# Kernel tuning notes

Hardware: AMD Instinct MI355X
Metric: run time of the kernel (lower is better)

Reference implementation:

```python
import jax, jax.numpy as jnp
import numpy as np

B, T, D = 4, 2048, 1024
E, K = 8, 2
H = int(D * 2.0)  # d_hidden


def setup_inputs() -> dict:
    key = jax.random.key(0)
    ks = jax.random.split(key, 7)
    x = jax.random.normal(ks[0], (B, T, D), dtype=jnp.float32)
    # router Linear(d_model, n_experts)
    router_w = jax.random.normal(ks[1], (D, E), dtype=jnp.float32) * (1.0 / np.sqrt(D))
    router_b = jnp.zeros((E,), dtype=jnp.float32)
    # expert weights, xavier_uniform-like scale
    lim1 = float(np.sqrt(6.0 / (D + H)))
    lim2 = float(np.sqrt(6.0 / (H + D)))
    w1 = jax.random.uniform(ks[2], (E, D, H), dtype=jnp.float32, minval=-lim1, maxval=lim1)
    b1 = jnp.zeros((E, H), dtype=jnp.float32)
    w2 = jax.random.uniform(ks[3], (E, H, D), dtype=jnp.float32, minval=-lim2, maxval=lim2)
    b2 = jnp.zeros((E, D), dtype=jnp.float32)
    return {"x": x, "router_w": router_w, "router_b": router_b,
            "w1": w1, "b1": b1, "w2": w2, "b2": b2}


def reference(x, router_w, router_b, w1, b1, w2, b2):
    Bs, Ts, d = x.shape
    N = Bs * Ts
    h = x.reshape(N, d)
    logits = h @ router_w + router_b                      # [N, E]
    probs = jax.nn.softmax(logits, axis=-1)
    weights, indices = jax.lax.top_k(probs, K)            # [N, K]
    weights = weights / (jnp.sum(weights, axis=-1, keepdims=True) + 1e-9)
    rows = jnp.arange(N)[:, None]
    # routing mask M and combine weights G (scatter over expert axis)
    M = jnp.zeros((N, E), dtype=bool).at[rows, indices].set(True)
    G = jnp.zeros((N, E), dtype=x.dtype).at[rows, indices].add(weights)
    # dense expert compute; tokens with G[:,e]==0 contribute nothing,
    # matching the masked gather/scatter loop exactly (dropout=0, eval mode)
    hidden = jax.nn.gelu(jnp.einsum('nd,edh->enh', h, w1) + b1[:, None, :],
                         approximate=False)               # [E, N, H]
    expert_out = jnp.einsum('enh,ehd->end', hidden, w2) + b2[:, None, :]  # [E, N, D]
    y = jnp.einsum('ne,end->nd', G, expert_out)           # combine
    y = y.reshape(Bs, Ts, d)
    # aux losses
    f_e = M.astype(jnp.float32).mean(axis=0)
    P_e = probs.mean(axis=0)
    lb_loss = -E * jnp.sum(f_e * P_e)
    z = jax.nn.logsumexp(logits, axis=-1)
    z_loss = jnp.mean(z ** 2)
    entropy = jnp.mean(-jnp.sum(probs * jnp.log(probs + 1e-10), axis=-1))
    return (y, lb_loss, z_loss, entropy, f_e, P_e)
```

## Files before the change

### kernel.cpp

```cpp
#include <hip/hip_runtime.h>
#include <hip/hip_bf16.h>

#define NTOK 8192
#define DM 1024
#define NE 8
#define DH 2048
#define CAP 18432

typedef __attribute__((ext_vector_type(8))) short short8;
typedef __attribute__((ext_vector_type(4))) float float4v;

#define ASYNC_COPY16(gsrc, ldst)                                                              \
    __builtin_amdgcn_global_load_lds((const __attribute__((address_space(1))) unsigned int*)(gsrc), \
                                     (__attribute__((address_space(3))) unsigned int*)(ldst), \
                                     16, 0, 0)

static __device__ __forceinline__ unsigned short f2bf(float f) {
    __hip_bfloat16 h = __float2bfloat16(f);
    return *reinterpret_cast<unsigned short*>(&h);
}

static __device__ __forceinline__ float fast_gelu(float v) {
    float x = v * 0.70710678118654752f;
    float ax = fabsf(x);
    float t = __frcp_rn(1.0f + 0.3275911f * ax);
    float poly = ((((1.061405429f * t - 1.453152027f) * t + 1.421413741f) * t
                   - 0.284496736f) * t + 0.254829592f) * t;
    float y = 1.0f - poly * __expf(-ax * ax);
    float erfv = copysignf(y, x);
    return 0.5f * v * (1.0f + erfv);
}


__global__ __launch_bounds__(256) void k_transpose(const float* __restrict__ src,
                                                   __hip_bfloat16* __restrict__ dst,
                                                   int R, int C) {
    __shared__ float t[64][65];
    size_t mat = (size_t)blockIdx.z * R * C;
    src += mat;
    dst += mat;
    int c0 = blockIdx.x * 64, r0 = blockIdx.y * 64;
    int tx = threadIdx.x & 63, ty = threadIdx.x >> 6;
#pragma unroll
    for (int i = 0; i < 16; i++) {
        int r = ty + i * 4;
        t[r][tx] = src[(size_t)(r0 + r) * C + c0 + tx];
    }
    __syncthreads();
    int rx = (threadIdx.x & 15) * 4;
    int cy = threadIdx.x >> 4;
#pragma unroll
    for (int i = 0; i < 4; i++) {
        int c = cy + i * 16;
        ushort4 v;
        v.x = f2bf(t[rx + 0][c]);
        v.y = f2bf(t[rx + 1][c]);
        v.z = f2bf(t[rx + 2][c]);
        v.w = f2bf(t[rx + 3][c]);
        *(ushort4*)((unsigned short*)dst + (size_t)(c0 + c) * R + r0 + rx) = v;
    }
}


__global__ __launch_bounds__(256) void k_router(const float* __restrict__ x,
                                                const float* __restrict__ rw,
                                                const float* __restrict__ rb,
                                                __hip_bfloat16* __restrict__ xb,
                                                int* __restrict__ topidx,
                                                float* __restrict__ topw,
                                                float* __restrict__ probs8,
                                                float* __restrict__ zent) {
    int lane = threadIdx.x & 63, wv = threadIdx.x >> 6;
    int n = blockIdx.x * 4 + wv;
    const float* xr = x + (size_t)n * DM;
    unsigned short* xbr = (unsigned short*)xb + (size_t)n * DM;
    float p[8] = {0.f, 0.f, 0.f, 0.f, 0.f, 0.f, 0.f, 0.f};
#pragma unroll
    for (int i = 0; i < 16; i++) {
        int d = lane + i * 64;
        float xv = xr[d];
        xbr[d] = f2bf(xv);
        const float4* w4 = (const float4*)(rw + (size_t)d * 8);
        float4 wa = w4[0], wb = w4[1];
        p[0] += xv * wa.x; p[1] += xv * wa.y; p[2] += xv * wa.z; p[3] += xv * wa.w;
        p[4] += xv * wb.x; p[5] += xv * wb.y; p[6] += xv * wb.z; p[7] += xv * wb.w;
    }
#pragma unroll
    for (int e = 0; e < 8; e++) {
#pragma unroll
        for (int off = 32; off > 0; off >>= 1) p[e] += __shfl_down(p[e], off);
    }
    if (lane == 0) {
        float logits[8], probs[8];
        float mx = -1e30f;
#pragma unroll
        for (int e = 0; e < 8; e++) {
            logits[e] = p[e] + rb[e];
            mx = fmaxf(mx, logits[e]);
        }
        float se = 0.f;
#pragma unroll
        for (int e = 0; e < 8; e++) {
            probs[e] = __expf(logits[e] - mx);
            se += probs[e];
        }
        float inv = 1.f / se;
        float z = mx + logf(se);
        float ent = 0.f;
#pragma unroll
        for (int e = 0; e < 8; e++) {
            probs[e] *= inv;
            ent -= probs[e] * logf(probs[e] + 1e-10f);
        }
        int i0 = 0;
#pragma unroll
        for (int e = 1; e < 8; e++)
            if (probs[e] > probs[i0]) i0 = e;
        int i1 = (i0 == 0) ? 1 : 0;
#pragma unroll
        for (int e = 0; e < 8; e++)
            if (e != i0 && e != i1 && probs[e] > probs[i1]) i1 = e;
        float w0 = probs[i0], w1v = probs[i1];
        float s = w0 + w1v + 1e-9f;
        topidx[2 * n] = i0;
        topidx[2 * n + 1] = i1;
        topw[2 * n] = w0 / s;
        topw[2 * n + 1] = w1v / s;
        float* pr = probs8 + (size_t)n * 8;
#pragma unroll
        for (int e = 0; e < 8; e++) pr[e] = probs[e];
        zent[2 * n] = z * z;
        zent[2 * n + 1] = ent;
    }
}


__global__ __launch_bounds__(256) void k_stats(const int* __restrict__ topidx,
                                               const float* __restrict__ probs8,
                                               const float* __restrict__ zent,
                                               float* __restrict__ fcnt,
                                               float* __restrict__ sump,
                                               float* __restrict__ szent) {
    int n = blockIdx.x * 256 + threadIdx.x;
    float v[18];
    int e0 = topidx[2 * n], e1 = topidx[2 * n + 1];
#pragma unroll
    for (int e = 0; e < 8; e++) v[e] = (float)((e == e0) + (e == e1));
    const float4* p4 = (const float4*)(probs8 + (size_t)n * 8);
    float4 pa = p4[0], pb = p4[1];
    v[8] = pa.x; v[9] = pa.y; v[10] = pa.z; v[11] = pa.w;
    v[12] = pb.x; v[13] = pb.y; v[14] = pb.z; v[15] = pb.w;
    v[16] = zent[2 * n];
    v[17] = zent[2 * n + 1];
#pragma unroll
    for (int i = 0; i < 18; i++)
#pragma unroll
        for (int off = 32; off > 0; off >>= 1) v[i] += __shfl_down(v[i], off);
    __shared__ float part[4][18];
    int lane = threadIdx.x & 63, wv = threadIdx.x >> 6;
    if (lane == 0)
#pragma unroll
        for (int i = 0; i < 18; i++) part[wv][i] = v[i];
    __syncthreads();
    if (threadIdx.x == 0) {
#pragma unroll
        for (int i = 0; i < 18; i++) {
            float s = part[0][i] + part[1][i] + part[2][i] + part[3][i];
            if (i < 8) atomicAdd(&fcnt[i], s);
            else if (i < 16) atomicAdd(&sump[i - 8], s);
            else atomicAdd(&szent[i - 16], s);
        }
    }
}


__global__ void k_scan(const float* __restrict__ fcnt, int* __restrict__ offs) {
    if (threadIdx.x == 0 && blockIdx.x == 0) {
        int o = 0;
        for (int e = 0; e < NE; e++) {
            offs[e] = o;
            int c = (int)(fcnt[e] + 0.5f);
            o += (c + 255) & ~255;
        }
        offs[NE] = o;
    }
}

__global__ __launch_bounds__(256) void k_scatter(const int* __restrict__ topidx,
                                                 const float* __restrict__ topw,
                                                 const int* __restrict__ offs,
                                                 int* __restrict__ cnt2,
                                                 int* __restrict__ rowtok,
                                                 float* __restrict__ roww,
                                                 int* __restrict__ slot) {
    __shared__ int lcnt[8], lbase[8];
    int tid = threadIdx.x;
    if (tid < 8) lcnt[tid] = 0;
    __syncthreads();
    int n = blockIdx.x * 256 + tid;
    int e0 = topidx[2 * n], e1 = topidx[2 * n + 1];
    int p0 = atomicAdd(&lcnt[e0], 1);
    int p1 = atomicAdd(&lcnt[e1], 1);
    __syncthreads();
    if (tid < 8) lbase[tid] = atomicAdd(&cnt2[tid], lcnt[tid]);
    __syncthreads();
    int r0 = offs[e0] + lbase[e0] + p0;
    int r1 = offs[e1] + lbase[e1] + p1;
    rowtok[r0] = n; roww[r0] = topw[2 * n];     slot[2 * n] = r0;
    rowtok[r1] = n; roww[r1] = topw[2 * n + 1]; slot[2 * n + 1] = r1;
}


#define KT1 (DM / 32)

__global__ __launch_bounds__(512) void k_gemm1(const __hip_bfloat16* __restrict__ xb,
                                               const __hip_bfloat16* __restrict__ w1T,
                                               const float* __restrict__ b1,
                                               const int* __restrict__ rowtok,
                                               const int* __restrict__ offs,
                                               __hip_bfloat16* __restrict__ hid) {
    int bid = blockIdx.x;
    int ib = bid >> 3;
    int row0 = ((bid & 7) * 9 + (ib >> 3)) * 256;
    if (row0 >= offs[NE]) return;
    int h0 = (ib & 7) * 256;
    int e = 0;
    while (row0 >= offs[e + 1]) e++;
    int tid = threadIdx.x;

    __shared__ __align__(16) short lds[3][16384];

    int sr = tid >> 2;
    int pc = tid & 3;
    int ch = pc ^ ((sr >> 1) & 3);
    int t0 = rowtok[row0 + sr];
    int t1 = rowtok[row0 + 128 + sr];
    const short* aS0 = (const short*)xb + (size_t)(t0 < 0 ? 0 : t0) * DM + ch * 8;
    const short* aS1 = (const short*)xb + (size_t)(t1 < 0 ? 0 : t1) * DM + ch * 8;
    const short* bS0 = (const short*)w1T + ((size_t)e * DH + h0 + sr) * DM + ch * 8;
    const short* bS1 = (const short*)w1T + ((size_t)e * DH + h0 + 128 + sr) * DM + ch * 8;
    int ldo = sr * 32 + pc * 8;

    int lane = tid & 63, wv = tid >> 6;
    int wm = (wv >> 2) * 128, wn = (wv & 3) * 64;
    int quad = lane >> 4, l16 = lane & 15;
    int a_off[8], b_off[4];
#pragma unroll
    for (int mt = 0; mt < 8; mt++) {
        int r = wm + mt * 16 + l16;
        a_off[mt] = r * 32 + ((quad ^ ((r >> 1) & 3)) * 8);
    }
#pragma unroll
    for (int nt = 0; nt < 4; nt++) {
        int r = wn + nt * 16 + l16;
        b_off[nt] = 8192 + r * 32 + ((quad ^ ((r >> 1) & 3)) * 8);
    }
    float4v acc[8][4];
#pragma unroll
    for (int i = 0; i < 8; i++)
#pragma unroll
        for (int j = 0; j < 4; j++) {
            float4v z = {0.f, 0.f, 0.f, 0.f};
            acc[i][j] = z;
        }

    ASYNC_COPY16(aS0, &lds[0][ldo]);
    ASYNC_COPY16(aS1, &lds[0][4096 + ldo]);
    ASYNC_COPY16(bS0, &lds[0][8192 + ldo]);
    ASYNC_COPY16(bS1, &lds[0][12288 + ldo]);
    ASYNC_COPY16(aS0 + 32, &lds[1][ldo]);
    ASYNC_COPY16(aS1 + 32, &lds[1][4096 + ldo]);
    ASYNC_COPY16(bS0 + 32, &lds[1][8192 + ldo]);
    ASYNC_COPY16(bS1 + 32, &lds[1][12288 + ldo]);
    asm volatile("s_waitcnt vmcnt(4)" ::: "memory");
    asm volatile("s_barrier" ::: "memory");

    int bi = 0;
#pragma unroll 1
    for (int t = 0; t < KT1; ++t) {
        const short* Ab = &lds[bi][0];
        int sbi = bi + 2; if (sbi >= 3) sbi -= 3;
        int k2 = (t + 2) * 32;
        short8 bf[4], af[4];
#pragma unroll
        for (int nt = 0; nt < 4; nt++) bf[nt] = *(const short8*)(Ab + b_off[nt]);
#pragma unroll
        for (int mt = 0; mt < 4; mt++) af[mt] = *(const short8*)(Ab + a_off[mt]);
        if (t + 2 < KT1) {
            ASYNC_COPY16(aS0 + k2, &lds[sbi][ldo]);
            ASYNC_COPY16(bS0 + k2, &lds[sbi][8192 + ldo]);
        }
        asm volatile("s_barrier" ::: "memory");
        __builtin_amdgcn_sched_barrier(0);
        __builtin_amdgcn_s_setprio(1);
#pragma unroll
        for (int mt = 0; mt < 4; mt++)
#pragma unroll
            for (int nt = 0; nt < 4; nt++)
                acc[mt][nt] = __builtin_amdgcn_mfma_f32_16x16x32_bf16(af[mt], bf[nt], acc[mt][nt], 0, 0, 0);
        __builtin_amdgcn_s_setprio(0);
        __builtin_amdgcn_sched_barrier(0);
        asm volatile("s_barrier" ::: "memory");
#pragma unroll
        for (int mt = 0; mt < 4; mt++) af[mt] = *(const short8*)(Ab + a_off[4 + mt]);
        if (t + 2 < KT1) {
            ASYNC_COPY16(aS1 + k2, &lds[sbi][4096 + ldo]);
            ASYNC_COPY16(bS1 + k2, &lds[sbi][12288 + ldo]);
        }
        asm volatile("s_barrier" ::: "memory");
        __builtin_amdgcn_sched_barrier(0);
        __builtin_amdgcn_s_setprio(1);
#pragma unroll
        for (int mt = 0; mt < 4; mt++)
#pragma unroll
            for (int nt = 0; nt < 4; nt++)
                acc[4 + mt][nt] = __builtin_amdgcn_mfma_f32_16x16x32_bf16(af[mt], bf[nt], acc[4 + mt][nt], 0, 0, 0);
        __builtin_amdgcn_s_setprio(0);
        __builtin_amdgcn_sched_barrier(0);
        if (t + 2 < KT1) asm volatile("s_waitcnt vmcnt(4)" ::: "memory");
        else             asm volatile("s_waitcnt vmcnt(0)" ::: "memory");
        asm volatile("s_barrier" ::: "memory");
        bi++; if (bi == 3) bi = 0;
    }

    const float* b1e = b1 + (size_t)e * DH + h0;
#pragma unroll
    for (int mt = 0; mt < 8; mt++) {
#pragma unroll
        for (int nt = 0; nt < 4; nt++) {
            int rl = wm + mt * 16 + quad * 4;
            int cl = wn + nt * 16 + l16;
            float bias = b1e[cl];
#pragma unroll
            for (int r = 0; r < 4; r++) {
                float v = fast_gelu(acc[mt][nt][r] + bias);
                hid[(size_t)(row0 + rl + r) * DH + h0 + cl] = __float2bfloat16(v);
            }
        }
    }
}


#define KT2 (DH / 32)

__global__ __launch_bounds__(512) void k_gemm2(const __hip_bfloat16* __restrict__ hid,
                                               const __hip_bfloat16* __restrict__ w2T,
                                               const float* __restrict__ b2,
                                               const float* __restrict__ roww,
                                               const int* __restrict__ offs,
                                               float* __restrict__ outb) {
    int bid = blockIdx.x;
    int ib = bid >> 3;
    int row0 = ((bid & 7) * 9 + (ib >> 3)) * 256;
    if (row0 >= offs[NE]) return;
    int d0 = (ib & 7) * 128;
    int e = 0;
    while (row0 >= offs[e + 1]) e++;
    int tid = threadIdx.x;

    __shared__ __align__(16) short lds[3][12288];

    int sr = tid >> 2, pc = tid & 3;
    int ch = pc ^ ((sr >> 1) & 3);
    const short* aS0 = (const short*)hid + (size_t)(row0 + sr) * DH + ch * 8;
    const short* aS1 = (const short*)hid + (size_t)(row0 + 128 + sr) * DH + ch * 8;
    const short* bS  = (const short*)w2T + ((size_t)e * DM + d0 + sr) * DH + ch * 8;
    int ldo = sr * 32 + pc * 8;

    int lane = tid & 63, wv = tid >> 6;
    int wm = (wv >> 1) * 64, wn = (wv & 1) * 64;
    int quad = lane >> 4, l16 = lane & 15;
    int a_off[4], b_off[4];
#pragma unroll
    for (int mt = 0; mt < 4; mt++) {
        int r = wm + mt * 16 + l16;
        a_off[mt] = r * 32 + ((quad ^ ((r >> 1) & 3)) * 8);
    }
#pragma unroll
    for (int nt = 0; nt < 4; nt++) {
        int r = wn + nt * 16 + l16;
        b_off[nt] = 8192 + r * 32 + ((quad ^ ((r >> 1) & 3)) * 8);
    }
    float4v acc[4][4];
#pragma unroll
    for (int i = 0; i < 4; i++)
#pragma unroll
        for (int j = 0; j < 4; j++) {
            float4v z = {0.f, 0.f, 0.f, 0.f};
            acc[i][j] = z;
        }

    ASYNC_COPY16(aS0, &lds[0][ldo]);
    ASYNC_COPY16(aS1, &lds[0][4096 + ldo]);
    ASYNC_COPY16(bS,  &lds[0][8192 + ldo]);
    ASYNC_COPY16(aS0 + 32, &lds[1][ldo]);
    ASYNC_COPY16(aS1 + 32, &lds[1][4096 + ldo]);
    ASYNC_COPY16(bS + 32,  &lds[1][8192 + ldo]);
    asm volatile("s_waitcnt vmcnt(3)" ::: "memory");
    asm volatile("s_barrier" ::: "memory");

    int bi = 0;
#pragma unroll 1
    for (int t = 0; t < KT2; ++t) {
        const short* Ab = &lds[bi][0];
        int sbi = bi + 2; if (sbi >= 3) sbi -= 3;
        int k2 = (t + 2) * 32;
        short8 af[4], bf[4];
#pragma unroll
        for (int mt = 0; mt < 4; mt++) af[mt] = *(const short8*)(Ab + a_off[mt]);
#pragma unroll
        for (int nt = 0; nt < 4; nt++) bf[nt] = *(const short8*)(Ab + b_off[nt]);
        if (t + 2 < KT2) {
            ASYNC_COPY16(aS0 + k2, &lds[sbi][ldo]);
            ASYNC_COPY16(aS1 + k2, &lds[sbi][4096 + ldo]);
            ASYNC_COPY16(bS + k2,  &lds[sbi][8192 + ldo]);
        }
        asm volatile("s_barrier" ::: "memory");
        __builtin_amdgcn_sched_barrier(0);
        __builtin_amdgcn_s_setprio(1);
#pragma unroll
        for (int mt = 0; mt < 4; mt++)
#pragma unroll
            for (int nt = 0; nt < 4; nt++)
                acc[mt][nt] = __builtin_amdgcn_mfma_f32_16x16x32_bf16(af[mt], bf[nt], acc[mt][nt], 0, 0, 0);
        __builtin_amdgcn_s_setprio(0);
        __builtin_amdgcn_sched_barrier(0);
        if (t + 2 < KT2) asm volatile("s_waitcnt vmcnt(3)" ::: "memory");
        else             asm volatile("s_waitcnt vmcnt(0)" ::: "memory");
        asm volatile("s_barrier" ::: "memory");
        bi++; if (bi == 3) bi = 0;
    }

    const float* b2e = b2 + (size_t)e * DM + d0;
#pragma unroll
    for (int mt = 0; mt < 4; mt++) {
#pragma unroll
        for (int nt = 0; nt < 4; nt++) {
            int rl = wm + mt * 16 + quad * 4;
            int cl = wn + nt * 16 + l16;
            float bias = b2e[cl];
#pragma unroll
            for (int r = 0; r < 4; r++) {
                int grow = row0 + rl + r;
                float v = (acc[mt][nt][r] + bias) * roww[grow];
                outb[(size_t)grow * DM + d0 + cl] = v;
            }
        }
    }
}


__global__ __launch_bounds__(256) void k_combine(const float* __restrict__ outb,
                                                 const int* __restrict__ slot,
                                                 float* __restrict__ y) {
    int n = blockIdx.x;
    int r0 = slot[2 * n], r1 = slot[2 * n + 1];
    const float4* p0 = (const float4*)(outb + (size_t)r0 * DM);
    const float4* p1 = (const float4*)(outb + (size_t)r1 * DM);
    float4 a = p0[threadIdx.x], b = p1[threadIdx.x];
    float4 c;
    c.x = a.x + b.x;
    c.y = a.y + b.y;
    c.z = a.z + b.z;
    c.w = a.w + b.w;
    ((float4*)(y + (size_t)n * DM))[threadIdx.x] = c;
}

__global__ void k_finalize(const float* __restrict__ fcnt, const float* __restrict__ sump,
                           const float* __restrict__ szent, float* __restrict__ out) {
    if (threadIdx.x == 0 && blockIdx.x == 0) {
        const float invN = 1.0f / (float)NTOK;
        float lb = 0.f;
        float f[NE], P[NE];
        for (int e = 0; e < NE; e++) {
            f[e] = fcnt[e] * invN;
            P[e] = sump[e] * invN;
            lb += f[e] * P[e];
        }
        size_t base = (size_t)NTOK * DM;
        out[base + 0] = -(float)NE * lb;
        out[base + 1] = szent[0] * invN;
        out[base + 2] = szent[1] * invN;
        for (int e = 0; e < NE; e++) out[base + 3 + e] = f[e];
        for (int e = 0; e < NE; e++) out[base + 11 + e] = P[e];
    }
}


extern "C" void kernel_launch(void* const* d_in, const int* in_sizes, int n_in,
                              void* d_out, int out_size, void* d_ws, size_t ws_size,
                              hipStream_t stream) {
    const float* x  = (const float*)d_in[0];
    const float* rw = (const float*)d_in[1];
    const float* rb = (const float*)d_in[2];
    const float* w1 = (const float*)d_in[3];
    const float* b1 = (const float*)d_in[4];
    const float* w2 = (const float*)d_in[5];
    const float* b2 = (const float*)d_in[6];
    float* out = (float*)d_out;

    char* ws = (char*)d_ws;
    size_t o = 0;
    auto alloc = [&](size_t bytes) {
        size_t r = o;
        o = (o + bytes + 255) & ~(size_t)255;
        return r;
    };
    __hip_bfloat16* w1T = (__hip_bfloat16*)(ws + alloc((size_t)NE * DM * DH * 2));
    __hip_bfloat16* w2T = (__hip_bfloat16*)(ws + alloc((size_t)NE * DM * DH * 2));
    __hip_bfloat16* xb  = (__hip_bfloat16*)(ws + alloc((size_t)NTOK * DM * 2));
    __hip_bfloat16* hid = (__hip_bfloat16*)(ws + alloc((size_t)CAP * DH * 2));
    float* outb = (float*)(ws + alloc((size_t)CAP * DM * 4));
    int* rowtok = (int*)(ws + alloc(CAP * 4));
    size_t zstart = o;
    float* roww  = (float*)(ws + alloc(CAP * 4));
    float* fcnt  = (float*)(ws + alloc(64));
    int* cnt2    = (int*)(ws + alloc(64));
    int* offs    = (int*)(ws + alloc(64));
    float* sump  = (float*)(ws + alloc(64));
    float* szent = (float*)(ws + alloc(64));
    size_t zend = o;
    int* topidx = (int*)(ws + alloc((size_t)NTOK * 2 * 4));
    float* topw = (float*)(ws + alloc((size_t)NTOK * 2 * 4));
    int* slot   = (int*)(ws + alloc((size_t)NTOK * 2 * 4));
    float* probs8 = (float*)(ws + alloc((size_t)NTOK * 8 * 4));
    float* zent   = (float*)(ws + alloc((size_t)NTOK * 2 * 4));

    hipMemsetAsync(rowtok, 0xFF, (size_t)CAP * 4, stream);
    hipMemsetAsync(ws + zstart, 0, zend - zstart, stream);

    k_transpose<<<dim3(DH / 64, DM / 64, NE), 256, 0, stream>>>(w1, w1T, DM, DH);
    k_transpose<<<dim3(DM / 64, DH / 64, NE), 256, 0, stream>>>(w2, w2T, DH, DM);
    k_router<<<NTOK / 4, 256, 0, stream>>>(x, rw, rb, xb, topidx, topw, probs8, zent);
    k_stats<<<NTOK / 256, 256, 0, stream>>>(topidx, probs8, zent, fcnt, sump, szent);
    k_scan<<<1, 1, 0, stream>>>(fcnt, offs);
    k_scatter<<<NTOK / 256, 256, 0, stream>>>(topidx, topw, offs, cnt2, rowtok, roww, slot);
    k_gemm1<<<576, 512, 0, stream>>>(xb, w1T, b1, rowtok, offs, hid);
    k_gemm2<<<576, 512, 0, stream>>>(hid, w2T, b2, roww, offs, outb);
    k_combine<<<NTOK, 256, 0, stream>>>(outb, slot, out);
    k_finalize<<<1, 1, 0, stream>>>(fcnt, sump, szent, out);
}
```

Before: 466.8 us.

## Fuse expert combine into gemm2 via atomic adds and retile gemm1 to 256x128

Measured after the change: 496.1 us. 1.06x slower.

```diff
diff --git a/kernel.cpp b/kernel.cpp
--- a/kernel.cpp
+++ b/kernel.cpp
@@ -191,8 +191,7 @@
                                                  const int* __restrict__ offs,
                                                  int* __restrict__ cnt2,
                                                  int* __restrict__ rowtok,
-                                                 float* __restrict__ roww,
-                                                 int* __restrict__ slot) {
+                                                 float* __restrict__ roww) {
     __shared__ int lcnt[8], lbase[8];
     int tid = threadIdx.x;
     if (tid < 8) lcnt[tid] = 0;
@@ -206,8 +205,8 @@
     __syncthreads();
     int r0 = offs[e0] + lbase[e0] + p0;
     int r1 = offs[e1] + lbase[e1] + p1;
-    rowtok[r0] = n; roww[r0] = topw[2 * n];     slot[2 * n] = r0;
-    rowtok[r1] = n; roww[r1] = topw[2 * n + 1]; slot[2 * n + 1] = r1;
+    rowtok[r0] = n; roww[r0] = topw[2 * n];
+    rowtok[r1] = n; roww[r1] = topw[2 * n + 1];
 }
 
 
@@ -221,32 +220,34 @@
                                                __hip_bfloat16* __restrict__ hid) {
     int bid = blockIdx.x;
     int ib = bid >> 3;
-    int row0 = ((bid & 7) * 9 + (ib >> 3)) * 256;
+    int row0 = ((bid & 7) * 9 + (ib >> 4)) * 256;
     if (row0 >= offs[NE]) return;
-    int h0 = (ib & 7) * 256;
+    int h0 = (ib & 15) * 128;
     int e = 0;
     while (row0 >= offs[e + 1]) e++;
     int tid = threadIdx.x;
 
-    __shared__ __align__(16) short lds[3][16384];
-
-    int sr = tid >> 2;
-    int pc = tid & 3;
+    __shared__ __align__(16) short lds[3][12288];
+    __shared__ int tokoff[256];
+    if (tid < 256) {
+        int t = rowtok[row0 + tid];
+        tokoff[tid] = (t < 0 ? 0 : t) * DM;
+    }
+    __syncthreads();
+
+    int sr = tid >> 2, pc = tid & 3;
     int ch = pc ^ ((sr >> 1) & 3);
-    int t0 = rowtok[row0 + sr];
-    int t1 = rowtok[row0 + 128 + sr];
-    const short* aS0 = (const short*)xb + (size_t)(t0 < 0 ? 0 : t0) * DM + ch * 8;
-    const short* aS1 = (const short*)xb + (size_t)(t1 < 0 ? 0 : t1) * DM + ch * 8;
-    const short* bS0 = (const short*)w1T + ((size_t)e * DH + h0 + sr) * DM + ch * 8;
-    const short* bS1 = (const short*)w1T + ((size_t)e * DH + h0 + 128 + sr) * DM + ch * 8;
+    const short* aS0 = (const short*)xb + tokoff[sr] + ch * 8;
+    const short* aS1 = (const short*)xb + tokoff[128 + sr] + ch * 8;
+    const short* bS  = (const short*)w1T + ((size_t)e * DH + h0 + sr) * DM + ch * 8;
     int ldo = sr * 32 + pc * 8;
 
     int lane = tid & 63, wv = tid >> 6;
-    int wm = (wv >> 2) * 128, wn = (wv & 3) * 64;
+    int wm = (wv >> 1) * 64, wn = (wv & 1) * 64;
     int quad = lane >> 4, l16 = lane & 15;
-    int a_off[8], b_off[4];
-#pragma unroll
-    for (int mt = 0; mt < 8; mt++) {
+    int a_off[4], b_off[4];
+#pragma unroll
+    for (int mt = 0; mt < 4; mt++) {
         int r = wm + mt * 16 + l16;
         a_off[mt] = r * 32 + ((quad ^ ((r >> 1) & 3)) * 8);
     }
@@ -255,9 +256,9 @@
         int r = wn + nt * 16 + l16;
         b_off[nt] = 8192 + r * 32 + ((quad ^ ((r >> 1) & 3)) * 8);
     }
-    float4v acc[8][4];
-#pragma unroll
-    for (int i = 0; i < 8; i++)
+    float4v acc[4][4];
+#pragma unroll
+    for (int i = 0; i < 4; i++)
 #pragma unroll
         for (int j = 0; j < 4; j++) {
             float4v z = {0.f, 0.f, 0.f, 0.f};
@@ -266,13 +267,11 @@
 
     ASYNC_COPY16(aS0, &lds[0][ldo]);
     ASYNC_COPY16(aS1, &lds[0][4096 + ldo]);
-    ASYNC_COPY16(bS0, &lds[0][8192 + ldo]);
-    ASYNC_COPY16(bS1, &lds[0][12288 + ldo]);
+    ASYNC_COPY16(bS,  &lds[0][8192 + ldo]);
     ASYNC_COPY16(aS0 + 32, &lds[1][ldo]);
     ASYNC_COPY16(aS1 + 32, &lds[1][4096 + ldo]);
-    ASYNC_COPY16(bS0 + 32, &lds[1][8192 + ldo]);
-    ASYNC_COPY16(bS1 + 32, &lds[1][12288 + ldo]);
-    asm volatile("s_waitcnt vmcnt(4)" ::: "memory");
+    ASYNC_COPY16(bS + 32,  &lds[1][8192 + ldo]);
+    asm volatile("s_waitcnt vmcnt(3)" ::: "memory");
     asm volatile("s_barrier" ::: "memory");
 
     int bi = 0;
@@ -281,17 +280,16 @@
         const short* Ab = &lds[bi][0];
         int sbi = bi + 2; if (sbi >= 3) sbi -= 3;
         int k2 = (t + 2) * 32;
-        short8 bf[4], af[4];
+        short8 af[4], bf[4];
+#pragma unroll
+        for (int mt = 0; mt < 4; mt++) af[mt] = *(const short8*)(Ab + a_off[mt]);
 #pragma unroll
         for (int nt = 0; nt < 4; nt++) bf[nt] = *(const short8*)(Ab + b_off[nt]);
-#pragma unroll
-        for (int mt = 0; mt < 4; mt++) af[mt] = *(const short8*)(Ab + a_off[mt]);
         if (t + 2 < KT1) {
             ASYNC_COPY16(aS0 + k2, &lds[sbi][ldo]);
-            ASYNC_COPY16(bS0 + k2, &lds[sbi][8192 + ldo]);
-        }
-        asm volatile("s_barrier" ::: "memory");
-        __builtin_amdgcn_sched_barrier(0);
+            ASYNC_COPY16(aS1 + k2, &lds[sbi][4096 + ldo]);
+            ASYNC_COPY16(bS + k2,  &lds[sbi][8192 + ldo]);
+        }
         __builtin_amdgcn_s_setprio(1);
 #pragma unroll
         for (int mt = 0; mt < 4; mt++)
@@ -299,25 +297,7 @@
             for (int nt = 0; nt < 4; nt++)
                 acc[mt][nt] = __builtin_amdgcn_mfma_f32_16x16x32_bf16(af[mt], bf[nt], acc[mt][nt], 0, 0, 0);
         __builtin_amdgcn_s_setprio(0);
-        __builtin_amdgcn_sched_barrier(0);
-        asm volatile("s_barrier" ::: "memory");
-#pragma unroll
-        for (int mt = 0; mt < 4; mt++) af[mt] = *(const short8*)(Ab + a_off[4 + mt]);
-        if (t + 2 < KT1) {
-            ASYNC_COPY16(aS1 + k2, &lds[sbi][4096 + ldo]);
-            ASYNC_COPY16(bS1 + k2, &lds[sbi][12288 + ldo]);
-        }
-        asm volatile("s_barrier" ::: "memory");
-        __builtin_amdgcn_sched_barrier(0);
-        __builtin_amdgcn_s_setprio(1);
-#pragma unroll
-        for (int mt = 0; mt < 4; mt++)
-#pragma unroll
-            for (int nt = 0; nt < 4; nt++)
-                acc[4 + mt][nt] = __builtin_amdgcn_mfma_f32_16x16x32_bf16(af[mt], bf[nt], acc[4 + mt][nt], 0, 0, 0);
-        __builtin_amdgcn_s_setprio(0);
-        __builtin_amdgcn_sched_barrier(0);
-        if (t + 2 < KT1) asm volatile("s_waitcnt vmcnt(4)" ::: "memory");
+        if (t + 2 < KT1) asm volatile("s_waitcnt vmcnt(3)" ::: "memory");
         else             asm volatile("s_waitcnt vmcnt(0)" ::: "memory");
         asm volatile("s_barrier" ::: "memory");
         bi++; if (bi == 3) bi = 0;
@@ -325,7 +305,7 @@
 
     const float* b1e = b1 + (size_t)e * DH + h0;
 #pragma unroll
-    for (int mt = 0; mt < 8; mt++) {
+    for (int mt = 0; mt < 4; mt++) {
 #pragma unroll
         for (int nt = 0; nt < 4; nt++) {
             int rl = wm + mt * 16 + quad * 4;
@@ -347,8 +327,9 @@
                                                const __hip_bfloat16* __restrict__ w2T,
                                                const float* __restrict__ b2,
                                                const float* __restrict__ roww,
+                                               const int* __restrict__ rowtok,
                                                const int* __restrict__ offs,
-                                               float* __restrict__ outb) {
+                                               float* __restrict__ y) {
     int bid = blockIdx.x;
     int ib = bid >> 3;
     int row0 = ((bid & 7) * 9 + (ib >> 3)) * 256;
@@ -359,6 +340,13 @@
     int tid = threadIdx.x;
 
     __shared__ __align__(16) short lds[3][12288];
+    __shared__ int tok_s[256];
+    __shared__ float rw_s[256];
+    if (tid < 256) {
+        tok_s[tid] = rowtok[row0 + tid];
+        rw_s[tid] = roww[row0 + tid];
+    }
+    __syncthreads();
 
     int sr = tid >> 2, pc = tid & 3;
     int ch = pc ^ ((sr >> 1) & 3);
@@ -415,8 +403,6 @@
             ASYNC_COPY16(aS1 + k2, &lds[sbi][4096 + ldo]);
             ASYNC_COPY16(bS + k2,  &lds[sbi][8192 + ldo]);
         }
-        asm volatile("s_barrier" ::: "memory");
-        __builtin_amdgcn_sched_barrier(0);
         __builtin_amdgcn_s_setprio(1);
 #pragma unroll
         for (int mt = 0; mt < 4; mt++)
@@ -424,7 +410,6 @@
             for (int nt = 0; nt < 4; nt++)
                 acc[mt][nt] = __builtin_amdgcn_mfma_f32_16x16x32_bf16(af[mt], bf[nt], acc[mt][nt], 0, 0, 0);
         __builtin_amdgcn_s_setprio(0);
-        __builtin_amdgcn_sched_barrier(0);
         if (t + 2 < KT2) asm volatile("s_waitcnt vmcnt(3)" ::: "memory");
         else             asm volatile("s_waitcnt vmcnt(0)" ::: "memory");
         asm volatile("s_barrier" ::: "memory");
@@ -441,30 +426,17 @@
             float bias = b2e[cl];
 #pragma unroll
             for (int r = 0; r < 4; r++) {
-                int grow = row0 + rl + r;
-                float v = (acc[mt][nt][r] + bias) * roww[grow];
-                outb[(size_t)grow * DM + d0 + cl] = v;
+                int lr = rl + r;
+                int tk = tok_s[lr];
+                if (tk >= 0) {
+                    float v = (acc[mt][nt][r] + bias) * rw_s[lr];
+                    atomicAdd(&y[(size_t)tk * DM + d0 + cl], v);
+                }
             }
         }
     }
 }
 
-
-__global__ __launch_bounds__(256) void k_combine(const float* __restrict__ outb,
-                                                 const int* __restrict__ slot,
-                                                 float* __restrict__ y) {
-    int n = blockIdx.x;
-    int r0 = slot[2 * n], r1 = slot[2 * n + 1];
-    const float4* p0 = (const float4*)(outb + (size_t)r0 * DM);
-    const float4* p1 = (const float4*)(outb + (size_t)r1 * DM);
-    float4 a = p0[threadIdx.x], b = p1[threadIdx.x];
-    float4 c;
-    c.x = a.x + b.x;
-    c.y = a.y + b.y;
-    c.z = a.z + b.z;
-    c.w = a.w + b.w;
-    ((float4*)(y + (size_t)n * DM))[threadIdx.x] = c;
-}
 
 __global__ void k_finalize(const float* __restrict__ fcnt, const float* __restrict__ sump,
                            const float* __restrict__ szent, float* __restrict__ out) {
@@ -510,7 +482,6 @@
     __hip_bfloat16* w2T = (__hip_bfloat16*)(ws + alloc((size_t)NE * DM * DH * 2));
     __hip_bfloat16* xb  = (__hip_bfloat16*)(ws + alloc((size_t)NTOK * DM * 2));
     __hip_bfloat16* hid = (__hip_bfloat16*)(ws + alloc((size_t)CAP * DH * 2));
-    float* outb = (float*)(ws + alloc((size_t)CAP * DM * 4));
     int* rowtok = (int*)(ws + alloc(CAP * 4));
     size_t zstart = o;
     float* roww  = (float*)(ws + alloc(CAP * 4));
@@ -522,21 +493,20 @@
     size_t zend = o;
     int* topidx = (int*)(ws + alloc((size_t)NTOK * 2 * 4));
     float* topw = (float*)(ws + alloc((size_t)NTOK * 2 * 4));
-    int* slot   = (int*)(ws + alloc((size_t)NTOK * 2 * 4));
     float* probs8 = (float*)(ws + alloc((size_t)NTOK * 8 * 4));
     float* zent   = (float*)(ws + alloc((size_t)NTOK * 2 * 4));
 
     hipMemsetAsync(rowtok, 0xFF, (size_t)CAP * 4, stream);
     hipMemsetAsync(ws + zstart, 0, zend - zstart, stream);
+    hipMemsetAsync(out, 0, (size_t)NTOK * DM * 4, stream);
 
     k_transpose<<<dim3(DH / 64, DM / 64, NE), 256, 0, stream>>>(w1, w1T, DM, DH);
     k_transpose<<<dim3(DM / 64, DH / 64, NE), 256, 0, stream>>>(w2, w2T, DH, DM);
     k_router<<<NTOK / 4, 256, 0, stream>>>(x, rw, rb, xb, topidx, topw, probs8, zent);
     k_stats<<<NTOK / 256, 256, 0, stream>>>(topidx, probs8, zent, fcnt, sump, szent);
     k_scan<<<1, 1, 0, stream>>>(fcnt, offs);
-    k_scatter<<<NTOK / 256, 256, 0, stream>>>(topidx, topw, offs, cnt2, rowtok, roww, slot);
-    k_gemm1<<<576, 512, 0, stream>>>(xb, w1T, b1, rowtok, offs, hid);
-    k_gemm2<<<576, 512, 0, stream>>>(hid, w2T, b2, roww, offs, outb);
-    k_combine<<<NTOK, 256, 0, stream>>>(outb, slot, out);
+    k_scatter<<<NTOK / 256, 256, 0, stream>>>(topidx, topw, offs, cnt2, rowtok, roww);
+    k_gemm1<<<1152, 512, 0, stream>>>(xb, w1T, b1, rowtok, offs, hid);
+    k_gemm2<<<576, 512, 0, stream>>>(hid, w2T, b2, roww, rowtok, offs, out);
     k_finalize<<<1, 1, 0, stream>>>(fcnt, sump, szent, out);
 }
```

## Restructure expert GEMM1 mainloop to BK=64 double-buffered with four-phase MFMA schedule

Applied to the files above, without the earlier changes.

Result: slower. 518.6 us (+11.1%).

```diff
diff --git a/kernel.cpp b/kernel.cpp
--- a/kernel.cpp
+++ b/kernel.cpp
@@ -211,7 +211,7 @@
 }
 
 
-#define KT1 (DM / 32)
+#define KT1 (DM / 64)
 
 __global__ __launch_bounds__(512) void k_gemm1(const __hip_bfloat16* __restrict__ xb,
                                                const __hip_bfloat16* __restrict__ w1T,
@@ -228,33 +228,39 @@
     while (row0 >= offs[e + 1]) e++;
     int tid = threadIdx.x;
 
-    __shared__ __align__(16) short lds[3][16384];
-
-    int sr = tid >> 2;
-    int pc = tid & 3;
-    int ch = pc ^ ((sr >> 1) & 3);
-    int t0 = rowtok[row0 + sr];
-    int t1 = rowtok[row0 + 128 + sr];
-    const short* aS0 = (const short*)xb + (size_t)(t0 < 0 ? 0 : t0) * DM + ch * 8;
-    const short* aS1 = (const short*)xb + (size_t)(t1 < 0 ? 0 : t1) * DM + ch * 8;
-    const short* bS0 = (const short*)w1T + ((size_t)e * DH + h0 + sr) * DM + ch * 8;
-    const short* bS1 = (const short*)w1T + ((size_t)e * DH + h0 + 128 + sr) * DM + ch * 8;
-    int ldo = sr * 32 + pc * 8;
+    __shared__ __align__(16) short lds[2][32768];
+    __shared__ int tokoff[256];
+    if (tid < 256) {
+        int t = rowtok[row0 + tid];
+        tokoff[tid] = (t < 0 ? 0 : t) * DM;
+    }
+    __syncthreads();
+    short* ldsw = &lds[0][0];
+
+    int r1 = tid >> 3, pch = tid & 7;
+    int lch = pch ^ (r1 & 7);
+    const short* aP00 = (const short*)xb + tokoff[r1] + lch * 8;
+    const short* aP01 = (const short*)xb + tokoff[r1 + 64] + lch * 8;
+    const short* aP10 = (const short*)xb + tokoff[r1 + 128] + lch * 8;
+    const short* aP11 = (const short*)xb + tokoff[r1 + 192] + lch * 8;
+    const short* bB   = (const short*)w1T + ((size_t)e * DH + h0) * DM + lch * 8;
+    const short* bP00 = bB + (size_t)r1 * DM;
+    const short* bP01 = bB + (size_t)(r1 + 64) * DM;
+    const short* bP10 = bB + (size_t)(r1 + 128) * DM;
+    const short* bP11 = bB + (size_t)(r1 + 192) * DM;
+
+    auto stage2 = [&](const short* s0, const short* s1, int kt, int dstS) {
+        ASYNC_COPY16(s0 + kt * 64, ldsw + dstS + tid * 8);
+        ASYNC_COPY16(s1 + kt * 64, ldsw + dstS + 4096 + tid * 8);
+    };
 
     int lane = tid & 63, wv = tid >> 6;
     int wm = (wv >> 2) * 128, wn = (wv & 3) * 64;
     int quad = lane >> 4, l16 = lane & 15;
-    int a_off[8], b_off[4];
-#pragma unroll
-    for (int mt = 0; mt < 8; mt++) {
-        int r = wm + mt * 16 + l16;
-        a_off[mt] = r * 32 + ((quad ^ ((r >> 1) & 3)) * 8);
-    }
-#pragma unroll
-    for (int nt = 0; nt < 4; nt++) {
-        int r = wn + nt * 16 + l16;
-        b_off[nt] = 8192 + r * 32 + ((quad ^ ((r >> 1) & 3)) * 8);
-    }
+    int ba = (wm + l16) * 64;
+    int bbs = 16384 + (wn + l16) * 64;
+    int x0 = (quad ^ (l16 & 7)) * 8;
+    int x1 = ((quad ^ (l16 & 7)) ^ 4) * 8;
     float4v acc[8][4];
 #pragma unroll
     for (int i = 0; i < 8; i++)
@@ -264,64 +270,142 @@
             acc[i][j] = z;
         }
 
-    ASYNC_COPY16(aS0, &lds[0][ldo]);
-    ASYNC_COPY16(aS1, &lds[0][4096 + ldo]);
-    ASYNC_COPY16(bS0, &lds[0][8192 + ldo]);
-    ASYNC_COPY16(bS1, &lds[0][12288 + ldo]);
-    ASYNC_COPY16(aS0 + 32, &lds[1][ldo]);
-    ASYNC_COPY16(aS1 + 32, &lds[1][4096 + ldo]);
-    ASYNC_COPY16(bS0 + 32, &lds[1][8192 + ldo]);
-    ASYNC_COPY16(bS1 + 32, &lds[1][12288 + ldo]);
+    stage2(aP00, aP01, 0, 0);
+    stage2(aP10, aP11, 0, 8192);
+    stage2(bP00, bP01, 0, 16384);
+    stage2(bP10, bP11, 0, 24576);
+    stage2(aP00, aP01, 1, 32768);
+    stage2(aP10, aP11, 1, 32768 + 8192);
     asm volatile("s_waitcnt vmcnt(4)" ::: "memory");
     asm volatile("s_barrier" ::: "memory");
 
-    int bi = 0;
+#define PH_ENTER                                            \
+    asm volatile("s_barrier" ::: "memory");                 \
+    asm volatile("s_waitcnt lgkmcnt(0)" ::: "memory");      \
+    __builtin_amdgcn_sched_barrier(0);                      \
+    __builtin_amdgcn_s_setprio(1);
+#define PH_EXIT                                             \
+    __builtin_amdgcn_s_setprio(0);                          \
+    __builtin_amdgcn_sched_barrier(0);                      \
+    asm volatile("s_barrier" ::: "memory");
+
 #pragma unroll 1
-    for (int t = 0; t < KT1; ++t) {
-        const short* Ab = &lds[bi][0];
-        int sbi = bi + 2; if (sbi >= 3) sbi -= 3;
-        int k2 = (t + 2) * 32;
-        short8 bf[4], af[4];
-#pragma unroll
-        for (int nt = 0; nt < 4; nt++) bf[nt] = *(const short8*)(Ab + b_off[nt]);
-#pragma unroll
-        for (int mt = 0; mt < 4; mt++) af[mt] = *(const short8*)(Ab + a_off[mt]);
-        if (t + 2 < KT1) {
-            ASYNC_COPY16(aS0 + k2, &lds[sbi][ldo]);
-            ASYNC_COPY16(bS0 + k2, &lds[sbi][8192 + ldo]);
-        }
-        asm volatile("s_barrier" ::: "memory");
-        __builtin_amdgcn_sched_barrier(0);
-        __builtin_amdgcn_s_setprio(1);
-#pragma unroll
-        for (int mt = 0; mt < 4; mt++)
-#pragma unroll
-            for (int nt = 0; nt < 4; nt++)
-                acc[mt][nt] = __builtin_amdgcn_mfma_f32_16x16x32_bf16(af[mt], bf[nt], acc[mt][nt], 0, 0, 0);
-        __builtin_amdgcn_s_setprio(0);
-        __builtin_amdgcn_sched_barrier(0);
-        asm volatile("s_barrier" ::: "memory");
-#pragma unroll
-        for (int mt = 0; mt < 4; mt++) af[mt] = *(const short8*)(Ab + a_off[4 + mt]);
-        if (t + 2 < KT1) {
-            ASYNC_COPY16(aS1 + k2, &lds[sbi][4096 + ldo]);
-            ASYNC_COPY16(bS1 + k2, &lds[sbi][12288 + ldo]);
-        }
-        asm volatile("s_barrier" ::: "memory");
-        __builtin_amdgcn_sched_barrier(0);
-        __builtin_amdgcn_s_setprio(1);
-#pragma unroll
-        for (int mt = 0; mt < 4; mt++)
-#pragma unroll
-            for (int nt = 0; nt < 4; nt++)
-                acc[4 + mt][nt] = __builtin_amdgcn_mfma_f32_16x16x32_bf16(af[mt], bf[nt], acc[4 + mt][nt], 0, 0, 0);
-        __builtin_amdgcn_s_setprio(0);
-        __builtin_amdgcn_sched_barrier(0);
-        if (t + 2 < KT1) asm volatile("s_waitcnt vmcnt(4)" ::: "memory");
-        else             asm volatile("s_waitcnt vmcnt(0)" ::: "memory");
-        asm volatile("s_barrier" ::: "memory");
-        bi++; if (bi == 3) bi = 0;
-    }
+    for (int it = 0; it < KT1 / 2; ++it) {
+        int t1 = 2 * it + 1, tn = 2 * it + 2;
+        bool more = tn < KT1;
+        short8 a0[8], a1[8], bq0, bq1;
+
+        {
+            const short* pa0 = ldsw + ba + x0;
+            const short* pa1 = ldsw + ba + x1;
+            const short* pb0 = ldsw + bbs + x0;
+            const short* pb1 = ldsw + bbs + x1;
+#pragma unroll
+            for (int mt = 0; mt < 8; mt++) a0[mt] = *(const short8*)(pa0 + mt * 1024);
+            bq0 = *(const short8*)(pb0);
+            bq1 = *(const short8*)(pb0 + 1024);
+            stage2(bP00, bP01, t1, 32768 + 16384);
+            PH_ENTER
+#pragma unroll
+            for (int mt = 0; mt < 8; mt++) {
+                acc[mt][0] = __builtin_amdgcn_mfma_f32_16x16x32_bf16(a0[mt], bq0, acc[mt][0], 0, 0, 0);
+                acc[mt][1] = __builtin_amdgcn_mfma_f32_16x16x32_bf16(a0[mt], bq1, acc[mt][1], 0, 0, 0);
+            }
+            PH_EXIT
+#pragma unroll
+            for (int mt = 0; mt < 8; mt++) a1[mt] = *(const short8*)(pa1 + mt * 1024);
+            bq0 = *(const short8*)(pb0 + 2048);
+            bq1 = *(const short8*)(pb0 + 3072);
+            stage2(bP10, bP11, t1, 32768 + 24576);
+            PH_ENTER
+#pragma unroll
+            for (int mt = 0; mt < 8; mt++) {
+                acc[mt][2] = __builtin_amdgcn_mfma_f32_16x16x32_bf16(a0[mt], bq0, acc[mt][2], 0, 0, 0);
+                acc[mt][3] = __builtin_amdgcn_mfma_f32_16x16x32_bf16(a0[mt], bq1, acc[mt][3], 0, 0, 0);
+            }
+            PH_EXIT
+            bq0 = *(const short8*)(pb1);
+            bq1 = *(const short8*)(pb1 + 1024);
+            if (more) stage2(aP00, aP01, tn, 0);
+            PH_ENTER
+#pragma unroll
+            for (int mt = 0; mt < 8; mt++) {
+                acc[mt][0] = __builtin_amdgcn_mfma_f32_16x16x32_bf16(a1[mt], bq0, acc[mt][0], 0, 0, 0);
+                acc[mt][1] = __builtin_amdgcn_mfma_f32_16x16x32_bf16(a1[mt], bq1, acc[mt][1], 0, 0, 0);
+            }
+            PH_EXIT
+            bq0 = *(const short8*)(pb1 + 2048);
+            bq1 = *(const short8*)(pb1 + 3072);
+            if (more) stage2(aP10, aP11, tn, 8192);
+            PH_ENTER
+#pragma unroll
+            for (int mt = 0; mt < 8; mt++) {
+                acc[mt][2] = __builtin_amdgcn_mfma_f32_16x16x32_bf16(a1[mt], bq0, acc[mt][2], 0, 0, 0);
+                acc[mt][3] = __builtin_amdgcn_mfma_f32_16x16x32_bf16(a1[mt], bq1, acc[mt][3], 0, 0, 0);
+            }
+            __builtin_amdgcn_s_setprio(0);
+            __builtin_amdgcn_sched_barrier(0);
+            if (more) asm volatile("s_waitcnt vmcnt(4)" ::: "memory");
+            else      asm volatile("s_waitcnt vmcnt(0)" ::: "memory");
+            asm volatile("s_barrier" ::: "memory");
+        }
+        {
+            const short* pa0 = ldsw + 32768 + ba + x0;
+            const short* pa1 = ldsw + 32768 + ba + x1;
+            const short* pb0 = ldsw + 32768 + bbs + x0;
+            const short* pb1 = ldsw + 32768 + bbs + x1;
+#pragma unroll
+            for (int mt = 0; mt < 8; mt++) a0[mt] = *(const short8*)(pa0 + mt * 1024);
+            bq0 = *(const short8*)(pb0);
+            bq1 = *(const short8*)(pb0 + 1024);
+            if (more) stage2(bP00, bP01, tn, 16384);
+            PH_ENTER
+#pragma unroll
+            for (int mt = 0; mt < 8; mt++) {
+                acc[mt][0] = __builtin_amdgcn_mfma_f32_16x16x32_bf16(a0[mt], bq0, acc[mt][0], 0, 0, 0);
+                acc[mt][1] = __builtin_amdgcn_mfma_f32_16x16x32_bf16(a0[mt], bq1, acc[mt][1], 0, 0, 0);
+            }
+            PH_EXIT
+#pragma unroll
+            for (int mt = 0; mt < 8; mt++) a1[mt] = *(const short8*)(pa1 + mt * 1024);
+            bq0 = *(const short8*)(pb0 + 2048);
+            bq1 = *(const short8*)(pb0 + 3072);
+            if (more) stage2(bP10, bP11, tn, 24576);
+            PH_ENTER
+#pragma unroll
+            for (int mt = 0; mt < 8; mt++) {
+                acc[mt][2] = __builtin_amdgcn_mfma_f32_16x16x32_bf16(a0[mt], bq0, acc[mt][2], 0, 0, 0);
+                acc[mt][3] = __builtin_amdgcn_mfma_f32_16x16x32_bf16(a0[mt], bq1, acc[mt][3], 0, 0, 0);
+            }
+            PH_EXIT
+            bq0 = *(const short8*)(pb1);
+            bq1 = *(const short8*)(pb1 + 1024);
+            if (more) stage2(aP00, aP01, tn + 1, 32768);
+            PH_ENTER
+#pragma unroll
+            for (int mt = 0; mt < 8; mt++) {
+                acc[mt][0] = __builtin_amdgcn_mfma_f32_16x16x32_bf16(a1[mt], bq0, acc[mt][0], 0, 0, 0);
+                acc[mt][1] = __builtin_amdgcn_mfma_f32_16x16x32_bf16(a1[mt], bq1, acc[mt][1], 0, 0, 0);
+            }
+            PH_EXIT
+            bq0 = *(const short8*)(pb1 + 2048);
+            bq1 = *(const short8*)(pb1 + 3072);
+            if (more) stage2(aP10, aP11, tn + 1, 32768 + 8192);
+            PH_ENTER
+#pragma unroll
+            for (int mt = 0; mt < 8; mt++) {
+                acc[mt][2] = __builtin_amdgcn_mfma_f32_16x16x32_bf16(a1[mt], bq0, acc[mt][2], 0, 0, 0);
+                acc[mt][3] = __builtin_amdgcn_mfma_f32_16x16x32_bf16(a1[mt], bq1, acc[mt][3], 0, 0, 0);
+            }
+            __builtin_amdgcn_s_setprio(0);
+            __builtin_amdgcn_sched_barrier(0);
+            if (more) asm volatile("s_waitcnt vmcnt(4)" ::: "memory");
+            else      asm volatile("s_waitcnt vmcnt(0)" ::: "memory");
+            asm volatile("s_barrier" ::: "memory");
+        }
+    }
+#undef PH_ENTER
+#undef PH_EXIT
 
     const float* b1e = b1 + (size_t)e * DH + h0;
 #pragma unroll
```
